# Kernel optimization log

Measured on AMD Instinct MI355X. Metric: run time of the kernel, lower is better.

## Reference

```python
import jax, jax.numpy as jnp
import numpy as np

BATCH, TOK, DIM, OUT = 4, 2048, 4096, 4096
E, R, TOP_K = 8, 16, 2
SCALING = 16.0 / R  # lora_alpha / r


def setup_inputs() -> dict:
    key = jax.random.key(0)
    ks = jax.random.split(key, 6)
    return {
        "x": jax.random.normal(ks[0], (BATCH, TOK, DIM), dtype=jnp.float32),
        "W_base": jax.random.normal(ks[1], (OUT, DIM), dtype=jnp.float32) / np.sqrt(DIM),
        "b_base": jax.random.normal(ks[2], (OUT,), dtype=jnp.float32) * 0.01,
        "W_gate": jax.random.normal(ks[3], (E, DIM), dtype=jnp.float32) * 0.01,
        "A": jax.random.normal(ks[4], (E, R, DIM), dtype=jnp.float32) / np.sqrt(DIM),
        "B": jax.random.normal(ks[5], (OUT, OUT // OUT * R * 0 + R), dtype=jnp.float32)[None].repeat(E, 0) * 0.0 + jax.random.normal(ks[5], (E, OUT, R), dtype=jnp.float32) * 0.02,
    }


def reference(x, W_base, b_base, W_gate, A, B):
    # Base frozen linear: [B,N,D] @ [D,O] -> [B,N,O]
    result = jnp.einsum("bnd,od->bno", x, W_base) + b_base
    # Gating
    logits = jnp.einsum("bnd,ed->bne", x, W_gate)
    probs = jax.nn.softmax(logits.astype(jnp.float32), axis=-1)  # fp32 softmax
    top_p, top_i = jax.lax.top_k(probs, TOP_K)  # [B,N,K]
    top_p = top_p / jnp.sum(top_p, axis=-1, keepdims=True)  # top_k > 1 branch
    top_p = top_p.astype(x.dtype)
    # Scatter top-k probs back to dense [B,N,E] routing weights
    route_w = jnp.sum(jax.nn.one_hot(top_i, E, dtype=x.dtype) * top_p[..., None], axis=-2)
    # Per-expert LoRA: down-project all tokens for all experts (r is small),
    # weight by routing, then up-project and sum over experts.
    h = jnp.einsum("bnd,erd->bner", x, A)          # [B,N,E,r]
    hw = h * route_w[..., None]                      # mask/combine weighting
    delta = jnp.einsum("bner,eor->bno", hw, B)      # [B,N,O]
    return result + delta * SCALING
```

## Files before the change

### kernel.cpp

```cpp
#include <hip/hip_runtime.h>
#include <hip/hip_bf16.h>
#include <cstdint>

#define TOKENS 8192
#define DIM_   4096
#define OUTD   4096
#define NE     8
#define NR     16
#define LORA_COLS (NE*NR)
#define KCAT  (DIM_ + LORA_COLS)
#define NTILES (KCAT/64)
#define HSPLIT 8
#define HKC    (DIM_/HSPLIT)

typedef __attribute__((ext_vector_type(8))) short short8;
typedef __attribute__((ext_vector_type(4))) float f32x4;

__device__ __forceinline__ unsigned short f2bf(float f) {
  union { float f; unsigned u; } v; v.f = f;
  unsigned r = v.u + 0x7FFFu + ((v.u >> 16) & 1u);
  return (unsigned short)(r >> 16);
}

__device__ __forceinline__ void load_lds16(const void* g, void* l) {
  auto gp = reinterpret_cast<const __attribute__((address_space(1))) unsigned int*>(
      reinterpret_cast<uintptr_t>(g));
  auto lp = reinterpret_cast<__attribute__((address_space(3))) unsigned int*>(
      reinterpret_cast<uintptr_t>(l));
  __builtin_amdgcn_global_load_lds(gp, lp, 16, 0, 0);
}

#define BAR() asm volatile("s_barrier" ::: "memory")
#define LGKM(N) do { asm volatile("s_waitcnt lgkmcnt(" #N ")" ::: "memory"); \
                     __builtin_amdgcn_sched_barrier(0); } while (0)
#define VMW(N) asm volatile("s_waitcnt vmcnt(" #N ")" ::: "memory")

__global__ __launch_bounds__(256) void conv_w_kernel(
    const float* __restrict__ W, const float* __restrict__ Bm,
    const float* __restrict__ Am, unsigned short* __restrict__ Wcat,
    unsigned short* __restrict__ Acat, float scaling) {
  int b = blockIdx.x, tid = threadIdx.x;
  if (b < OUTD) {
    const float4* src = (const float4*)(W + (size_t)b * DIM_);
    unsigned short* dst = Wcat + (size_t)b * KCAT;
#pragma unroll
    for (int j = 0; j < DIM_ / 1024; ++j) {
      float4 v = src[j * 256 + tid];
      ushort4 o; o.x = f2bf(v.x); o.y = f2bf(v.y); o.z = f2bf(v.z); o.w = f2bf(v.w);
      *(ushort4*)(dst + (size_t)(j * 256 + tid) * 4) = o;
    }
    if (tid < LORA_COLS) {
      int e = tid >> 4, r = tid & 15;
      dst[DIM_ + tid] = f2bf(scaling * Bm[((size_t)e * OUTD + b) * NR + r]);
    }
  } else {
    int i = b - OUTD;
    const float4* src = (const float4*)(Am + (size_t)i * DIM_);
    unsigned short* dst = Acat + (size_t)i * DIM_;
#pragma unroll
    for (int j = 0; j < DIM_ / 1024; ++j) {
      float4 v = src[j * 256 + tid];
      ushort4 o; o.x = f2bf(v.x); o.y = f2bf(v.y); o.z = f2bf(v.z); o.w = f2bf(v.w);
      *(ushort4*)(dst + (size_t)(j * 256 + tid) * 4) = o;
    }
  }
}

__global__ __launch_bounds__(256) void prep_x_kernel(
    const float* __restrict__ x, const float* __restrict__ Wg,
    unsigned short* __restrict__ Xcat, int* __restrict__ ridx,
    float* __restrict__ rw) {
  __shared__ float red[32 * 257];
  __shared__ float lg[32];
  int tid = threadIdx.x;
  int t0 = blockIdx.x * 4;
  float acc[4][8];
#pragma unroll
  for (int ti = 0; ti < 4; ++ti)
#pragma unroll
    for (int e = 0; e < 8; ++e) acc[ti][e] = 0.f;
  const float4* x4 = (const float4*)x;
  const float4* wg4 = (const float4*)Wg;
#pragma unroll
  for (int j = 0; j < 4; ++j) {
    int dpos = j * 256 + tid;
    float4 wg[8];
#pragma unroll
    for (int e = 0; e < 8; ++e) wg[e] = wg4[e * 1024 + dpos];
#pragma unroll
    for (int ti = 0; ti < 4; ++ti) {
      float4 v = x4[(size_t)(t0 + ti) * 1024 + dpos];
      ushort4 o; o.x = f2bf(v.x); o.y = f2bf(v.y); o.z = f2bf(v.z); o.w = f2bf(v.w);
      *(ushort4*)&Xcat[(size_t)(t0 + ti) * KCAT + (size_t)dpos * 4] = o;
#pragma unroll
      for (int e = 0; e < 8; ++e)
        acc[ti][e] += v.x * wg[e].x + v.y * wg[e].y + v.z * wg[e].z + v.w * wg[e].w;
    }
  }
#pragma unroll
  for (int p = 0; p < 32; ++p) red[p * 257 + tid] = acc[p >> 3][p & 7];
  __syncthreads();
  {
    int p = tid >> 3, part = tid & 7;
    float s = 0.f;
#pragma unroll
    for (int i = 0; i < 32; ++i) s += red[p * 257 + part * 32 + i];
    s += __shfl_xor(s, 1);
    s += __shfl_xor(s, 2);
    s += __shfl_xor(s, 4);
    if (part == 0) lg[p] = s;
  }
  __syncthreads();
  if (tid < 4) {
    float l[8];
#pragma unroll
    for (int e = 0; e < 8; ++e) l[e] = lg[tid * 8 + e];
    int i0 = 0; float m0 = l[0];
#pragma unroll
    for (int e = 1; e < 8; ++e) if (l[e] > m0) { m0 = l[e]; i0 = e; }
    int i1 = -1; float m1 = -3.4e38f;
#pragma unroll
    for (int e = 0; e < 8; ++e) if (e != i0 && l[e] > m1) { m1 = l[e]; i1 = e; }
    float w0 = 1.0f / (1.0f + expf(m1 - m0));
    int t = t0 + tid;
    ridx[t * 2] = i0; ridx[t * 2 + 1] = i1;
    rw[t * 2] = w0;  rw[t * 2 + 1] = 1.0f - w0;
  }
}

template <int MODE>
__global__ __launch_bounds__(256) void gemm_kernel(
    const unsigned short* __restrict__ Aop, const unsigned short* __restrict__ Bop,
    float* __restrict__ Cout, unsigned short* __restrict__ CoutBf,
    const float* __restrict__ bias, const int* __restrict__ ridx,
    const float* __restrict__ rw,
    int M, int N, int K, int lda, int ldb, int ldc) {
  __shared__ __align__(16) unsigned short lsA[128 * 32];
  __shared__ __align__(16) unsigned short lsB[128 * 32];
  int tid = threadIdx.x;
  int lane = tid & 63, wave = tid >> 6;
  int wm = wave >> 1, wn = wave & 1;
  int row0 = blockIdx.x * 128, col0 = blockIdx.y * 128;

  f32x4 acc[4][4];
#pragma unroll
  for (int a = 0; a < 4; ++a)
#pragma unroll
    for (int b = 0; b < 4; ++b) acc[a][b] = (f32x4){0.f, 0.f, 0.f, 0.f};

  int lrow = lane >> 2;
  int lcol = (lane & 3) << 3;
  int fr = lane & 15, fk = (lane >> 4) << 3;

  const unsigned short* gA0 = Aop + (size_t)(row0 + wave * 32 + lrow) * lda + lcol;
  const unsigned short* gA1 = Aop + (size_t)(row0 + wave * 32 + 16 + lrow) * lda + lcol;
  const unsigned short* gB0 = Bop + (size_t)(col0 + wave * 32 + lrow) * ldb + lcol;
  const unsigned short* gB1 = Bop + (size_t)(col0 + wave * 32 + 16 + lrow) * ldb + lcol;

  for (int k0 = 0; k0 < K; k0 += 32) {
    load_lds16(gA0 + k0, lsA + wave * 1024);
    load_lds16(gA1 + k0, lsA + wave * 1024 + 512);
    load_lds16(gB0 + k0, lsB + wave * 1024);
    load_lds16(gB1 + k0, lsB + wave * 1024 + 512);
    __syncthreads();
    short8 af[4], bfr[4];
#pragma unroll
    for (int mi = 0; mi < 4; ++mi)
      af[mi] = *(const short8*)&lsA[(wm * 64 + mi * 16 + fr) * 32 + fk];
#pragma unroll
    for (int ni = 0; ni < 4; ++ni)
      bfr[ni] = *(const short8*)&lsB[(wn * 64 + ni * 16 + fr) * 32 + fk];
#pragma unroll
    for (int mi = 0; mi < 4; ++mi)
#pragma unroll
      for (int ni = 0; ni < 4; ++ni)
        acc[mi][ni] = __builtin_amdgcn_mfma_f32_16x16x32_bf16(af[mi], bfr[ni], acc[mi][ni], 0, 0, 0);
    __syncthreads();
  }

  int fg = lane >> 4;
  if (MODE == 0) {
#pragma unroll
    for (int ni = 0; ni < 4; ++ni) {
      int col = col0 + wn * 64 + ni * 16 + fr;
      float bv = bias[col];
#pragma unroll
      for (int mi = 0; mi < 4; ++mi)
#pragma unroll
        for (int j = 0; j < 4; ++j) {
          int row = row0 + wm * 64 + mi * 16 + fg * 4 + j;
          Cout[(size_t)row * ldc + col] = acc[mi][ni][j] + bv;
        }
    }
  } else {
#pragma unroll
    for (int mi = 0; mi < 4; ++mi)
#pragma unroll
      for (int j = 0; j < 4; ++j) {
        int row = row0 + wm * 64 + mi * 16 + fg * 4 + j;
        int i0 = ridx[row * 2], i1 = ridx[row * 2 + 1];
        float w0 = rw[row * 2], w1 = rw[row * 2 + 1];
#pragma unroll
        for (int ni = 0; ni < 4; ++ni) {
          int col = wn * 64 + ni * 16 + fr;
          int e = col >> 4;
          float w = (e == i0) ? w0 : ((e == i1) ? w1 : 0.f);
          CoutBf[(size_t)row * ldc + col] = f2bf(w * acc[mi][ni][j]);
        }
      }
  }
}

__global__ __launch_bounds__(256) void gemm_h_sk_kernel(
    const unsigned short* __restrict__ Aop,
    const unsigned short* __restrict__ Bop,
    float* __restrict__ Hpart) {
  __shared__ __align__(16) unsigned short lsA[128 * 32];
  __shared__ __align__(16) unsigned short lsB[128 * 32];
  int tid = threadIdx.x;
  int lane = tid & 63, wave = tid >> 6;
  int wm = wave >> 1, wn = wave & 1;
  int row0 = blockIdx.x * 128;
  int s = blockIdx.y;
  int kbeg = s * HKC;

  f32x4 acc[4][4];
#pragma unroll
  for (int a = 0; a < 4; ++a)
#pragma unroll
    for (int b = 0; b < 4; ++b) acc[a][b] = (f32x4){0.f, 0.f, 0.f, 0.f};

  int lrow = lane >> 2;
  int lcol = (lane & 3) << 3;
  int fr = lane & 15, fk = (lane >> 4) << 3;

  const unsigned short* gA0 = Aop + (size_t)(row0 + wave * 32 + lrow) * KCAT + lcol;
  const unsigned short* gA1 = Aop + (size_t)(row0 + wave * 32 + 16 + lrow) * KCAT + lcol;
  const unsigned short* gB0 = Bop + (size_t)(wave * 32 + lrow) * DIM_ + lcol;
  const unsigned short* gB1 = Bop + (size_t)(wave * 32 + 16 + lrow) * DIM_ + lcol;

  for (int k0 = kbeg; k0 < kbeg + HKC; k0 += 32) {
    load_lds16(gA0 + k0, lsA + wave * 1024);
    load_lds16(gA1 + k0, lsA + wave * 1024 + 512);
    load_lds16(gB0 + k0, lsB + wave * 1024);
    load_lds16(gB1 + k0, lsB + wave * 1024 + 512);
    __syncthreads();
    short8 af[4], bfr[4];
#pragma unroll
    for (int mi = 0; mi < 4; ++mi)
      af[mi] = *(const short8*)&lsA[(wm * 64 + mi * 16 + fr) * 32 + fk];
#pragma unroll
    for (int ni = 0; ni < 4; ++ni)
      bfr[ni] = *(const short8*)&lsB[(wn * 64 + ni * 16 + fr) * 32 + fk];
#pragma unroll
    for (int mi = 0; mi < 4; ++mi)
#pragma unroll
      for (int ni = 0; ni < 4; ++ni)
        acc[mi][ni] = __builtin_amdgcn_mfma_f32_16x16x32_bf16(af[mi], bfr[ni], acc[mi][ni], 0, 0, 0);
    __syncthreads();
  }

  int fg = lane >> 4;
  float* outp = Hpart + (size_t)s * TOKENS * 128;
#pragma unroll
  for (int ni = 0; ni < 4; ++ni) {
    int col = wn * 64 + ni * 16 + fr;
#pragma unroll
    for (int mi = 0; mi < 4; ++mi)
#pragma unroll
      for (int j = 0; j < 4; ++j) {
        int row = row0 + wm * 64 + mi * 16 + fg * 4 + j;
        outp[(size_t)row * 128 + col] = acc[mi][ni][j];
      }
  }
}

__global__ __launch_bounds__(256) void h_combine_kernel(
    const float* __restrict__ Hpart, const int* __restrict__ ridx,
    const float* __restrict__ rw, unsigned short* __restrict__ Xcat) {
  int gid = blockIdx.x * 256 + threadIdx.x;
  int t = gid >> 7, c = gid & 127;
  float s = 0.f;
#pragma unroll
  for (int i = 0; i < HSPLIT; ++i) s += Hpart[(size_t)i * TOKENS * 128 + gid];
  int e = c >> 4;
  int i0 = ridx[t * 2], i1 = ridx[t * 2 + 1];
  float w = (e == i0) ? rw[t * 2] : ((e == i1) ? rw[t * 2 + 1] : 0.f);
  Xcat[(size_t)t * KCAT + DIM_ + c] = f2bf(w * s);
}

#define RD_A4(dst, base, ks, mi0) do { \
  dst[0] = *(const short8*)((base) + (((mi0)+0)*2+(ks))*1024); \
  dst[1] = *(const short8*)((base) + (((mi0)+1)*2+(ks))*1024); \
  dst[2] = *(const short8*)((base) + (((mi0)+2)*2+(ks))*1024); \
  dst[3] = *(const short8*)((base) + (((mi0)+3)*2+(ks))*1024); } while (0)
#define RD_B4(dst, base, ks) do { \
  dst[0] = *(const short8*)((base) + 0*2048 + (ks)*1024); \
  dst[1] = *(const short8*)((base) + 1*2048 + (ks)*1024); \
  dst[2] = *(const short8*)((base) + 2*2048 + (ks)*1024); \
  dst[3] = *(const short8*)((base) + 3*2048 + (ks)*1024); } while (0)
#define MFMA_BLK(a4, b4, m0) do { \
  __builtin_amdgcn_s_setprio(1); \
  _Pragma("unroll") \
  for (int mi = 0; mi < 4; ++mi) { \
    _Pragma("unroll") \
    for (int ni = 0; ni < 4; ++ni) { \
      acc[(m0)+mi][ni] = __builtin_amdgcn_mfma_f32_16x16x32_bf16( \
          b4[ni], a4[mi], acc[(m0)+mi][ni], 0, 0, 0); } } \
  __builtin_amdgcn_s_setprio(0); } while (0)
#define STAGE(srcp, kofs, dst) do { \
  load_lds16((srcp) + (kofs), (dst)); \
  load_lds16((srcp) + (kofs) + 32, (dst) + 1024); } while (0)

__global__ __launch_bounds__(512, 2) void gemm256_kernel(
    const unsigned short* __restrict__ Aop,
    const unsigned short* __restrict__ Bop,
    float* __restrict__ Cout, const float* __restrict__ bias) {
  extern __shared__ char lds[];
  const int tid = threadIdx.x;
  const int lane = tid & 63, wave = tid >> 6;
  const int wm = wave >> 2, wn = wave & 3;
  const int fr = lane & 15, kg = lane >> 4;

  const int bid = blockIdx.x;
  const int swz = (bid & 7) * 64 + (bid >> 3);
  const int mt = swz >> 4, nt = swz & 15;
  const int row0 = mt * 256, col0 = nt * 256;

  const int srow = lane >> 2;
  const int scol = ((lane & 3) * 8) ^ (((lane >> 5) & 1) * 16);
  const unsigned short* sA0 = Aop + (size_t)(row0 +       wave * 16 + srow) * KCAT + scol;
  const unsigned short* sA1 = Aop + (size_t)(row0 + 128 + wave * 16 + srow) * KCAT + scol;
  const unsigned short* sB0 = Bop + (size_t)(col0 +       wave * 16 + srow) * KCAT + scol;
  const unsigned short* sB1 = Bop + (size_t)(col0 + 128 + wave * 16 + srow) * KCAT + scol;

  char* dA0b0 = lds +      0 + wave * 2048;
  char* dA1b0 = lds +  16384 + wave * 2048;
  char* dB0b0 = lds +  32768 + wave * 2048;
  char* dB1b0 = lds +  49152 + wave * 2048;
  char* dA0b1 = dA0b0 + 65536;
  char* dA1b1 = dA1b0 + 65536;
  char* dB0b1 = dB0b0 + 65536;
  char* dB1b1 = dB1b0 + 65536;

  const int swzo = (kg * 16) ^ ((fr >> 3) << 5);
  const char* rdA0 = lds + wm * 16384 + fr * 64 + swzo;
  const char* rdA1 = rdA0 + 65536;
  const char* rdB0 = lds + 32768 + (wn >> 1) * 16384 + (wn & 1) * 8192 + fr * 64 + swzo;
  const char* rdB1 = rdB0 + 65536;

  f32x4 acc[8][4];
#pragma unroll
  for (int a = 0; a < 8; ++a)
#pragma unroll
    for (int b = 0; b < 4; ++b) acc[a][b] = (f32x4){0.f, 0.f, 0.f, 0.f};

  short8 aL[4], aH[4], a1L[4], a1H[4], b0f[4], b1f[4];

  STAGE(sA0, 0, dA0b0); STAGE(sA1, 0, dA1b0);
  STAGE(sB0, 0, dB0b0); STAGE(sB1, 0, dB1b0);
  STAGE(sB0, 64, dB0b1); STAGE(sA0, 64, dA0b1);
  VMW(4);
  BAR();
  RD_A4(aL, rdA0, 0, 0); RD_B4(b0f, rdB0, 0);

  for (int i = 0; i < NTILES / 2 - 1; ++i) {
    const int k1 = (2 * i + 1) * 64, k2 = k1 + 64, k3 = k1 + 128;
    RD_A4(aH, rdA0, 0, 4); RD_B4(b1f, rdB0, 1);
    STAGE(sB1, k1, dB1b1);
    BAR(); LGKM(8);
    MFMA_BLK(aL, b0f, 0);
    BAR();
    RD_A4(a1L, rdA0, 1, 0);
    STAGE(sA1, k1, dA1b1);
    BAR(); LGKM(4);
    MFMA_BLK(aH, b0f, 4);
    BAR();
    RD_A4(a1H, rdA0, 1, 4);
    STAGE(sB0, k2, dB0b0);
    BAR(); LGKM(4);
    MFMA_BLK(a1L, b1f, 0);
    BAR();
    STAGE(sA0, k2, dA0b0);
    VMW(4);
    BAR();
    RD_A4(aL, rdA1, 0, 0); RD_B4(b0f, rdB1, 0);
    LGKM(8);
    MFMA_BLK(a1H, b1f, 4);
    BAR();
    RD_A4(aH, rdA1, 0, 4); RD_B4(b1f, rdB1, 1);
    STAGE(sB1, k2, dB1b0);
    BAR(); LGKM(8);
    MFMA_BLK(aL, b0f, 0);
    BAR();
    RD_A4(a1L, rdA1, 1, 0);
    STAGE(sA1, k2, dA1b0);
    BAR(); LGKM(4);
    MFMA_BLK(aH, b0f, 4);
    BAR();
    RD_A4(a1H, rdA1, 1, 4);
    STAGE(sB0, k3, dB0b1);
    BAR(); LGKM(4);
    MFMA_BLK(a1L, b1f, 0);
    BAR();
    STAGE(sA0, k3, dA0b1);
    VMW(4);
    BAR();
    RD_A4(aL, rdA0, 0, 0); RD_B4(b0f, rdB0, 0);
    LGKM(8);
    MFMA_BLK(a1H, b1f, 4);
    BAR();
  }

  {
    const int k65 = 65 * 64;
    RD_A4(aH, rdA0, 0, 4); RD_B4(b1f, rdB0, 1);
    STAGE(sB1, k65, dB1b1);
    BAR(); LGKM(8);
    MFMA_BLK(aL, b0f, 0);
    BAR();
    RD_A4(a1L, rdA0, 1, 0);
    STAGE(sA1, k65, dA1b1);
    BAR(); LGKM(4);
    MFMA_BLK(aH, b0f, 4);
    BAR();
    RD_A4(a1H, rdA0, 1, 4);
    BAR(); LGKM(4);
    MFMA_BLK(a1L, b1f, 0);
    BAR();
    VMW(0);
    BAR();
    RD_A4(aL, rdA1, 0, 0); RD_B4(b0f, rdB1, 0);
    LGKM(8);
    MFMA_BLK(a1H, b1f, 4);
    BAR();
    RD_A4(aH, rdA1, 0, 4); RD_B4(b1f, rdB1, 1);
    LGKM(8);
    MFMA_BLK(aL, b0f, 0);
    RD_A4(a1L, rdA1, 1, 0);
    LGKM(4);
    MFMA_BLK(aH, b0f, 4);
    RD_A4(a1H, rdA1, 1, 4);
    LGKM(4);
    MFMA_BLK(a1L, b1f, 0);
    LGKM(0);
    MFMA_BLK(a1H, b1f, 4);
  }

#pragma unroll
  for (int ni = 0; ni < 4; ++ni) {
    int colb = col0 + wn * 64 + ni * 16 + kg * 4;
    float4 bv = *(const float4*)&bias[colb];
#pragma unroll
    for (int mi = 0; mi < 8; ++mi) {
      int row = row0 + wm * 128 + mi * 16 + fr;
      float4 v;
      v.x = acc[mi][ni][0] + bv.x;
      v.y = acc[mi][ni][1] + bv.y;
      v.z = acc[mi][ni][2] + bv.z;
      v.w = acc[mi][ni][3] + bv.w;
      *(float4*)&Cout[(size_t)row * OUTD + colb] = v;
    }
  }
}

extern "C" void kernel_launch(void* const* d_in, const int* in_sizes, int n_in,
                              void* d_out, int out_size, void* d_ws, size_t ws_size,
                              hipStream_t stream) {
  const float* x  = (const float*)d_in[0];
  const float* Wb = (const float*)d_in[1];
  const float* bb = (const float*)d_in[2];
  const float* Wg = (const float*)d_in[3];
  const float* Am = (const float*)d_in[4];
  const float* Bm = (const float*)d_in[5];
  float* out = (float*)d_out;

  unsigned short* Wcat = (unsigned short*)d_ws;
  unsigned short* Xcat = Wcat + (size_t)OUTD * KCAT;
  unsigned short* Acat = Xcat + (size_t)TOKENS * KCAT;
  int*   ridx = (int*)(Acat + (size_t)LORA_COLS * DIM_);
  float* rw   = (float*)(ridx + (size_t)TOKENS * 2);
  float* Hpart = (float*)(rw + (size_t)TOKENS * 2);

  const size_t ws_needed = (size_t)((char*)(Hpart + (size_t)HSPLIT * TOKENS * 128)
                                    - (char*)d_ws);
  const bool use_splitk = (ws_size >= ws_needed);

  const float scaling = 16.0f / (float)NR;

  hipFuncSetAttribute((const void*)gemm256_kernel,
                      hipFuncAttributeMaxDynamicSharedMemorySize, 131072);

  conv_w_kernel<<<dim3(OUTD + LORA_COLS), dim3(256), 0, stream>>>(
      Wb, Bm, Am, Wcat, Acat, scaling);
  prep_x_kernel<<<dim3(TOKENS / 4), dim3(256), 0, stream>>>(
      x, Wg, Xcat, ridx, rw);
  if (use_splitk) {
    gemm_h_sk_kernel<<<dim3(TOKENS / 128, HSPLIT), dim3(256), 0, stream>>>(
        Xcat, Acat, Hpart);
    h_combine_kernel<<<dim3(TOKENS * 128 / 256), dim3(256), 0, stream>>>(
        Hpart, ridx, rw, Xcat);
  } else {
    gemm_kernel<1><<<dim3(TOKENS / 128, 1), dim3(256), 0, stream>>>(
        Xcat, Acat, (float*)nullptr, Xcat + DIM_, (const float*)nullptr,
        ridx, rw, TOKENS, LORA_COLS, DIM_, KCAT, DIM_, KCAT);
  }
  gemm256_kernel<<<dim3(512), dim3(512), 131072, stream>>>(Xcat, Wcat, out, bb);
}
```

Before: 319.8 us.

## Fuse weight and activation prep kernels; deepen GEMM prefetch to three stages in flight

Merges the weight-conversion and activation-prep kernels into one launch, with blocks dispatched by index range. This removes one kernel launch and lets the two memory-bound conversions run concurrently. Separately, the main GEMM's staging order is rotated so each global-to-LDS load is issued one slot earlier, with vmcnt waits raised from 4 to 6. That keeps more loads in flight to hide latency, but changes buffer reuse timing and risks a WAR hazard if the schedule is wrong. The fused kernel also reserves the gating shared memory for every block, which could lower occupancy for the conversion blocks.

```diff
diff --git a/kernel.cpp b/kernel.cpp
--- a/kernel.cpp
+++ b/kernel.cpp
@@ -35,14 +35,19 @@
                      __builtin_amdgcn_sched_barrier(0); } while (0)
 #define VMW(N) asm volatile("s_waitcnt vmcnt(" #N ")" ::: "memory")
 
-__global__ __launch_bounds__(256) void conv_w_kernel(
+__global__ __launch_bounds__(256) void fused_prep_kernel(
+    const float* __restrict__ x, const float* __restrict__ Wg,
     const float* __restrict__ W, const float* __restrict__ Bm,
     const float* __restrict__ Am, unsigned short* __restrict__ Wcat,
-    unsigned short* __restrict__ Acat, float scaling) {
-  int b = blockIdx.x, tid = threadIdx.x;
-  if (b < OUTD) {
-    const float4* src = (const float4*)(W + (size_t)b * DIM_);
-    unsigned short* dst = Wcat + (size_t)b * KCAT;
+    unsigned short* __restrict__ Acat, unsigned short* __restrict__ Xcat,
+    int* __restrict__ ridx, float* __restrict__ rw, float scaling) {
+  __shared__ float red[32 * 257];
+  __shared__ float lg[32];
+  int tid = threadIdx.x;
+  int bb = blockIdx.x;
+  if (bb < OUTD) {
+    const float4* src = (const float4*)(W + (size_t)bb * DIM_);
+    unsigned short* dst = Wcat + (size_t)bb * KCAT;
 #pragma unroll
     for (int j = 0; j < DIM_ / 1024; ++j) {
       float4 v = src[j * 256 + tid];
@@ -51,10 +56,12 @@
     }
     if (tid < LORA_COLS) {
       int e = tid >> 4, r = tid & 15;
-      dst[DIM_ + tid] = f2bf(scaling * Bm[((size_t)e * OUTD + b) * NR + r]);
+      dst[DIM_ + tid] = f2bf(scaling * Bm[((size_t)e * OUTD + bb) * NR + r]);
     }
-  } else {
-    int i = b - OUTD;
+    return;
+  }
+  if (bb < OUTD + LORA_COLS) {
+    int i = bb - OUTD;
     const float4* src = (const float4*)(Am + (size_t)i * DIM_);
     unsigned short* dst = Acat + (size_t)i * DIM_;
 #pragma unroll
@@ -63,17 +70,9 @@
       ushort4 o; o.x = f2bf(v.x); o.y = f2bf(v.y); o.z = f2bf(v.z); o.w = f2bf(v.w);
       *(ushort4*)(dst + (size_t)(j * 256 + tid) * 4) = o;
     }
-  }
-}
-
-__global__ __launch_bounds__(256) void prep_x_kernel(
-    const float* __restrict__ x, const float* __restrict__ Wg,
-    unsigned short* __restrict__ Xcat, int* __restrict__ ridx,
-    float* __restrict__ rw) {
-  __shared__ float red[32 * 257];
-  __shared__ float lg[32];
-  int tid = threadIdx.x;
-  int t0 = blockIdx.x * 4;
+    return;
+  }
+  int t0 = (bb - OUTD - LORA_COLS) * 4;
   float acc[4][8];
 #pragma unroll
   for (int ti = 0; ti < 4; ++ti)
@@ -359,52 +358,52 @@
 
   STAGE(sA0, 0, dA0b0); STAGE(sA1, 0, dA1b0);
   STAGE(sB0, 0, dB0b0); STAGE(sB1, 0, dB1b0);
-  STAGE(sB0, 64, dB0b1); STAGE(sA0, 64, dA0b1);
-  VMW(4);
+  STAGE(sB0, 64, dB0b1); STAGE(sB1, 64, dB1b1); STAGE(sA0, 64, dA0b1);
+  VMW(6);
   BAR();
   RD_A4(aL, rdA0, 0, 0); RD_B4(b0f, rdB0, 0);
 
   for (int i = 0; i < NTILES / 2 - 1; ++i) {
     const int k1 = (2 * i + 1) * 64, k2 = k1 + 64, k3 = k1 + 128;
     RD_A4(aH, rdA0, 0, 4); RD_B4(b1f, rdB0, 1);
-    STAGE(sB1, k1, dB1b1);
+    STAGE(sA1, k1, dA1b1);
     BAR(); LGKM(8);
     MFMA_BLK(aL, b0f, 0);
     BAR();
     RD_A4(a1L, rdA0, 1, 0);
-    STAGE(sA1, k1, dA1b1);
+    STAGE(sB0, k2, dB0b0);
     BAR(); LGKM(4);
     MFMA_BLK(aH, b0f, 4);
     BAR();
     RD_A4(a1H, rdA0, 1, 4);
-    STAGE(sB0, k2, dB0b0);
+    STAGE(sB1, k2, dB1b0);
     BAR(); LGKM(4);
     MFMA_BLK(a1L, b1f, 0);
     BAR();
     STAGE(sA0, k2, dA0b0);
-    VMW(4);
+    VMW(6);
     BAR();
     RD_A4(aL, rdA1, 0, 0); RD_B4(b0f, rdB1, 0);
     LGKM(8);
     MFMA_BLK(a1H, b1f, 4);
     BAR();
     RD_A4(aH, rdA1, 0, 4); RD_B4(b1f, rdB1, 1);
-    STAGE(sB1, k2, dB1b0);
+    STAGE(sA1, k2, dA1b0);
     BAR(); LGKM(8);
     MFMA_BLK(aL, b0f, 0);
     BAR();
     RD_A4(a1L, rdA1, 1, 0);
-    STAGE(sA1, k2, dA1b0);
+    STAGE(sB0, k3, dB0b1);
     BAR(); LGKM(4);
     MFMA_BLK(aH, b0f, 4);
     BAR();
     RD_A4(a1H, rdA1, 1, 4);
-    STAGE(sB0, k3, dB0b1);
+    STAGE(sB1, k3, dB1b1);
     BAR(); LGKM(4);
     MFMA_BLK(a1L, b1f, 0);
     BAR();
     STAGE(sA0, k3, dA0b1);
-    VMW(4);
+    VMW(6);
     BAR();
     RD_A4(aL, rdA0, 0, 0); RD_B4(b0f, rdB0, 0);
     LGKM(8);
@@ -415,12 +414,11 @@
   {
     const int k65 = 65 * 64;
     RD_A4(aH, rdA0, 0, 4); RD_B4(b1f, rdB0, 1);
-    STAGE(sB1, k65, dB1b1);
+    STAGE(sA1, k65, dA1b1);
     BAR(); LGKM(8);
     MFMA_BLK(aL, b0f, 0);
     BAR();
     RD_A4(a1L, rdA0, 1, 0);
-    STAGE(sA1, k65, dA1b1);
     BAR(); LGKM(4);
     MFMA_BLK(aH, b0f, 4);
     BAR();
@@ -491,10 +489,8 @@
   hipFuncSetAttribute((const void*)gemm256_kernel,
                       hipFuncAttributeMaxDynamicSharedMemorySize, 131072);
 
-  conv_w_kernel<<<dim3(OUTD + LORA_COLS), dim3(256), 0, stream>>>(
-      Wb, Bm, Am, Wcat, Acat, scaling);
-  prep_x_kernel<<<dim3(TOKENS / 4), dim3(256), 0, stream>>>(
-      x, Wg, Xcat, ridx, rw);
+  fused_prep_kernel<<<dim3(OUTD + LORA_COLS + TOKENS / 4), dim3(256), 0, stream>>>(
+      x, Wg, Wb, Bm, Am, Wcat, Acat, Xcat, ridx, rw, scaling);
   if (use_splitk) {
     gemm_h_sk_kernel<<<dim3(TOKENS / 128, HSPLIT), dim3(256), 0, stream>>>(
         Xcat, Acat, Hpart);
```

Measured after the change: 318.7 us, median of 2. Within noise of the previous version (-0.4%).
